# Kernel optimization log

Hardware: AMD Instinct MI355X
Metric: run time of the kernel (lower is better)

The kernel has to match this reference:

```python
import jax, jax.numpy as jnp
import numpy as np
from jax import lax

B, T, L = 256, 128, 64
E_ENC = 512   # encoder_hidden_size
D = 512       # decoder_hidden_size
EMB = 128     # action_embed_size
A = 129       # action_size + 1
ATT_H = 20    # attention MLP hidden width


def setup_inputs() -> dict:
    key = jax.random.key(0)
    ks = jax.random.split(key, 32)
    n = lambda k, shape, s=0.05: jax.random.normal(k, shape, jnp.float32) * s
    inp = {
        'padded_actions': jax.random.randint(ks[0], (B, T), 0, A),
        'sentence_encoding': jax.random.normal(ks[1], (B, L, E_ENC), jnp.float32),
        'enc_h': jax.random.normal(ks[2], (B, D), jnp.float32),
        'enc_c': jax.random.normal(ks[3], (B, D), jnp.float32),
        # embedding
        'emb_W': n(ks[4], (A, EMB)),
        # attn_combine: Linear(E_ENC+EMB -> D)  (cat order: [embed, ctx])
        'Wc': n(ks[5], (D, EMB + E_ENC)), 'bc': jnp.zeros((D,), jnp.float32),
        # three LSTMCells (torch layout: W_ih [4D, in], W_hh [4D, D])
        'Wih1': n(ks[6], (4 * D, D)), 'Whh1': n(ks[7], (4 * D, D)),
        'bih1': jnp.zeros((4 * D,), jnp.float32), 'bhh1': jnp.zeros((4 * D,), jnp.float32),
        'Wih2': n(ks[8], (4 * D, D)), 'Whh2': n(ks[9], (4 * D, D)),
        'bih2': jnp.zeros((4 * D,), jnp.float32), 'bhh2': jnp.zeros((4 * D,), jnp.float32),
        'Wih3': n(ks[10], (4 * D, D)), 'Whh3': n(ks[11], (4 * D, D)),
        'bih3': jnp.zeros((4 * D,), jnp.float32), 'bhh3': jnp.zeros((4 * D,), jnp.float32),
        # attention MLP: Linear(D+E_ENC -> 20), ReLU, Linear(20 -> 1), Tanh
        'Wa1': n(ks[12], (ATT_H, E_ENC + D)), 'ba1': jnp.zeros((ATT_H,), jnp.float32),
        'Wa2': n(ks[13], (1, ATT_H)), 'ba2': jnp.zeros((1,), jnp.float32),
        # action head: Linear(D+E_ENC -> D), ReLU, Linear(D -> A)
        'Wl1': n(ks[14], (D, D + E_ENC)), 'bl1': jnp.zeros((D,), jnp.float32),
        'Wl2': n(ks[15], (A, D)), 'bl2': jnp.zeros((A,), jnp.float32),
    }
    return inp


def _lstm_cell(x, h, c, Wih, Whh, bih, bhh):
    gates = x @ Wih.T + bih + h @ Whh.T + bhh  # [B, 4D]
    i, f, g, o = jnp.split(gates, 4, axis=-1)
    c_new = jax.nn.sigmoid(f) * c + jax.nn.sigmoid(i) * jnp.tanh(g)
    h_new = jax.nn.sigmoid(o) * jnp.tanh(c_new)
    return h_new, c_new


def reference(padded_actions, sentence_encoding, enc_h, enc_c, emb_W, Wc, bc,
              Wih1, Whh1, bih1, bhh1, Wih2, Whh2, bih2, bhh2, Wih3, Whh3, bih3, bhh3,
              Wa1, ba1, Wa2, ba2, Wl1, bl1, Wl2, bl2):
    bsz, tlen = padded_actions.shape
    lmax = sentence_encoding.shape[1]
    embed = emb_W[padded_actions]  # [B, T, EMB]
    # deterministic teacher forcing: embed_tm1 at t is embed[:, t-1], zeros at t=0
    emb_tm1_seq = jnp.concatenate(
        [jnp.zeros((bsz, 1, embed.shape[-1]), embed.dtype), embed[:, :-1]], axis=1)
    xs = jnp.swapaxes(emb_tm1_seq, 0, 1)  # [T, B, EMB]

    ctx0 = jnp.zeros((bsz, sentence_encoding.shape[-1]), jnp.float32)
    init = (enc_h, enc_c, enc_h, enc_c, enc_h, enc_c, ctx0)

    def step(carry, e_tm1):
        h0, c0, h1, c1, h2, c2, ctx = carry
        att_t = jnp.concatenate([e_tm1, ctx], axis=-1) @ Wc.T + bc  # attn_combine
        h0, c0 = _lstm_cell(att_t, h0, c0, Wih1, Whh1, bih1, bhh1)
        h1, c1 = _lstm_cell(h0, h1, c1, Wih2, Whh2, bih2, bhh2)
        h2, c2 = _lstm_cell(h1, h2, c2, Wih3, Whh3, bih3, bhh3)
        # attention over encoder outputs: cat(enc_out, h2) -> MLP -> tanh -> softmax
        h_rep = jnp.broadcast_to(h2[:, None, :], (bsz, lmax, h2.shape[-1]))
        feat = jnp.concatenate([sentence_encoding, h_rep], axis=-1)  # [B, L, E+D]
        score = jnp.tanh(jax.nn.relu(feat @ Wa1.T + ba1) @ Wa2.T + ba2)[..., 0]  # [B, L]
        w = jax.nn.softmax(score, axis=1)
        ctx_new = jnp.einsum('bl,ble->be', w, sentence_encoding)
        # action head on cat(h2, ctx)
        hw = jnp.concatenate([h2, ctx_new], axis=-1)
        logits = jax.nn.relu(hw @ Wl1.T + bl1) @ Wl2.T + bl2  # [B, A]
        return (h0, c0, h1, c1, h2, c2, ctx_new), logits

    _, logits_seq = lax.scan(step, init, xs)  # [T, B, A]
    logits = jnp.swapaxes(logits_seq, 0, 1).reshape(bsz * tlen, -1)
    return logits
```

## Files before the change

kernel.cpp:

```cpp
#include <hip/hip_runtime.h>
#include <math.h>

constexpr int BSZ  = 256;
constexpr int TLEN = 128;
constexpr int LLEN = 64;
constexpr int DH   = 512;
constexpr int EMBD = 128;
constexpr int ACTN = 129;
constexpr int HATT = 20;

typedef short bf16x8 __attribute__((ext_vector_type(8)));
typedef float f32x4  __attribute__((ext_vector_type(4)));

__device__ __forceinline__ short f2bf(float f) {
    unsigned u = __builtin_bit_cast(unsigned, f);
    u += 0x7fffu + ((u >> 16) & 1u);
    return (short)(u >> 16);
}
__device__ __forceinline__ float bf2f(short s) {
    unsigned u = ((unsigned)(unsigned short)s) << 16;
    return __builtin_bit_cast(float, u);
}

__launch_bounds__(256)
__global__ void k_fold(const float* __restrict__ Wih1, const float* __restrict__ Wc,
                       float* __restrict__ W1f)
{
    __shared__ float at[64][33];
    __shared__ float bt[32][65];
    int tid = threadIdx.x;
    int tx = tid & 15, ty = tid >> 4;
    int n0 = blockIdx.x * 64, k0 = blockIdx.y * 64;
    float acc[4][4] = {};
    for (int m0 = 0; m0 < 512; m0 += 32) {
        for (int i = 0; i < 8; ++i) {
            int idx = tid + 256 * i;
            int nl = idx >> 5, ml = idx & 31;
            at[nl][ml] = Wih1[(size_t)(n0 + nl) * 512 + m0 + ml];
        }
        for (int i = 0; i < 8; ++i) {
            int idx = tid + 256 * i;
            int ml = idx >> 6, kl = idx & 63;
            bt[ml][kl] = Wc[(size_t)(m0 + ml) * 640 + k0 + kl];
        }
        __syncthreads();
        for (int m = 0; m < 32; ++m) {
            #pragma unroll
            for (int i = 0; i < 4; ++i) {
                float av = at[ty * 4 + i][m];
                #pragma unroll
                for (int j = 0; j < 4; ++j)
                    acc[i][j] += av * bt[m][tx * 4 + j];
            }
        }
        __syncthreads();
    }
    for (int i = 0; i < 4; ++i)
        for (int j = 0; j < 4; ++j)
            W1f[(size_t)(n0 + ty * 4 + i) * 640 + (k0 + tx * 4 + j)] = acc[i][j];
}

__global__ void k_pack23(const float* __restrict__ Wih, const float* __restrict__ Whh,
                         short* __restrict__ pack)
{
    int idx = blockIdx.x * 256 + threadIdx.x;
    int lane = idx & 63;
    int ks = (idx >> 6) & 31;
    int nn = idx >> 11;
    int np = nn * 16 + (lane & 15);
    int k  = ks * 32 + ((lane >> 4) << 3);
    int n  = (np & 3) * 512 + (np >> 2);
    const float* src = (k < 512) ? (Wih + (size_t)n * 512 + k)
                                 : (Whh + (size_t)n * 512 + (k - 512));
    short* dst = pack + (size_t)idx * 8;
    #pragma unroll
    for (int i = 0; i < 8; ++i) dst[i] = f2bf(src[i]);
}

__global__ void k_pack1(const float* __restrict__ W1f, const float* __restrict__ Whh1,
                        short* __restrict__ pack)
{
    int idx = blockIdx.x * 256 + threadIdx.x;
    int lane = idx & 63;
    int tmp = idx >> 6;
    int ks = tmp % 36;
    int nn = tmp / 36;
    int np = nn * 16 + (lane & 15);
    int k  = ks * 32 + ((lane >> 4) << 3);
    int n  = (np & 3) * 512 + (np >> 2);
    const float* src = (k < 640) ? (W1f + (size_t)n * 640 + k)
                                 : (Whh1 + (size_t)n * 512 + (k - 640));
    short* dst = pack + (size_t)idx * 8;
    #pragma unroll
    for (int i = 0; i < 8; ++i) dst[i] = f2bf(src[i]);
}

__global__ void k_packh1(const float* __restrict__ Wl1, short* __restrict__ pack)
{
    int idx = blockIdx.x * 256 + threadIdx.x;
    int lane = idx & 63;
    int ks = (idx >> 6) & 31;
    int nn = idx >> 11;
    int np = nn * 16 + (lane & 15);
    int k  = ks * 32 + ((lane >> 4) << 3);
    const float* src = Wl1 + (size_t)np * 1024 + k;
    short* dst = pack + (size_t)idx * 8;
    #pragma unroll
    for (int i = 0; i < 8; ++i) dst[i] = f2bf(src[i]);
}

__global__ void k_packh2(const float* __restrict__ Wl2, short* __restrict__ pack)
{
    int idx = blockIdx.x * 256 + threadIdx.x;
    int lane = idx & 63;
    int ks = (idx >> 6) & 15;
    int nn = idx >> 10;
    int np = nn * 16 + (lane & 15);
    int k  = ks * 32 + ((lane >> 4) << 3);
    short* dst = pack + (size_t)idx * 8;
    if (np < ACTN) {
        const float* src = Wl2 + (size_t)np * 512 + k;
        #pragma unroll
        for (int i = 0; i < 8; ++i) dst[i] = f2bf(src[i]);
    } else {
        #pragma unroll
        for (int i = 0; i < 8; ++i) dst[i] = 0;
    }
}

__global__ void k_bias(const float* __restrict__ Wih1, const float* __restrict__ bc,
                       const float* bih1, const float* bhh1,
                       const float* bih2, const float* bhh2,
                       const float* bih3, const float* bhh3,
                       float* b1p, float* b2p, float* b3p)
{
    int cp = blockIdx.x * 256 + threadIdx.x;
    int n = (cp & 3) * 512 + (cp >> 2);
    float s = bih1[n] + bhh1[n];
    for (int m = 0; m < 512; ++m) s += Wih1[(size_t)n * 512 + m] * bc[m];
    b1p[cp] = s;
    b2p[cp] = bih2[n] + bhh2[n];
    b3p[cp] = bih3[n] + bhh3[n];
}

__global__ void k_tr(float* __restrict__ dst, const float* __restrict__ src,
                     int R, int C, int sld, int dld)
{
    int idx = blockIdx.x * 256 + threadIdx.x;
    if (idx >= R * C) return;
    int c = idx / R, r = idx - c * R;
    dst[c * dld + r] = src[r * sld + c];
}

__launch_bounds__(256)
__global__ void k_encp(const float* __restrict__ enc, const float* __restrict__ Wa1,
                       const float* __restrict__ ba1, float* __restrict__ ENCP)
{
    __shared__ float wa[HATT * 513];
    __shared__ float er[8][513];
    int b = blockIdx.x, tid = threadIdx.x;
    for (int idx = tid; idx < HATT * 512; idx += 256) {
        int h = idx >> 9, e = idx & 511;
        wa[h * 513 + e] = Wa1[h * 1024 + e];
    }
    __syncthreads();
    for (int c = 0; c < 8; ++c) {
        for (int i = 0; i < 16; ++i) {
            int idx = tid + 256 * i;
            int rr = idx >> 9, e = idx & 511;
            er[rr][e] = enc[((size_t)b * LLEN + c * 8 + rr) * 512 + e];
        }
        __syncthreads();
        if (tid < 8 * HATT) {
            int rr = tid & 7, h = tid >> 3;
            float s = 0.f;
            for (int e = 0; e < 512; ++e) s += er[rr][e] * wa[h * 513 + e];
            ENCP[((size_t)b * LLEN + c * 8 + rr) * HATT + h] = s + ba1[h];
        }
        __syncthreads();
    }
}

__global__ void k_embed(const int* __restrict__ act, const float* __restrict__ embW,
                        short* __restrict__ ET)
{
    int idx = blockIdx.x * 256 + threadIdx.x;
    int t = idx >> 15;
    int rem = idx & 32767;
    int b = rem >> 7, k = rem & 127;
    float v = 0.f;
    if (t > 0) v = embW[(size_t)act[b * TLEN + t - 1] * EMBD + k];
    ET[idx] = f2bf(v);
}

__global__ void k_encb(const float* __restrict__ enc, short* __restrict__ ENCB)
{
    int i = blockIdx.x * 256 + threadIdx.x;
    float4 v = *(const float4*)&enc[(size_t)i * 4];
    short4 o;
    o.x = f2bf(v.x); o.y = f2bf(v.y); o.z = f2bf(v.z); o.w = f2bf(v.w);
    *(short4*)&ENCB[(size_t)i * 4] = o;
}

__global__ void k_init(const float* __restrict__ eh,
                       short* h0, short* h1, short* h2, short* ctx)
{
    int i = blockIdx.x * 256 + threadIdx.x;
    short hb = f2bf(eh[i]);
    h0[i] = hb; h1[i] = hb; h2[i] = hb; ctx[i] = 0;
}

__device__ __forceinline__ void load_a8(const short* base,
    bf16x8& a0, bf16x8& a1, bf16x8& a2, bf16x8& a3,
    bf16x8& a4, bf16x8& a5, bf16x8& a6, bf16x8& a7)
{
    asm volatile(
        "global_load_dwordx4 %0, %8, off sc0\n\t"
        "global_load_dwordx4 %1, %8, off offset:64 sc0\n\t"
        "global_load_dwordx4 %2, %8, off offset:128 sc0\n\t"
        "global_load_dwordx4 %3, %8, off offset:192 sc0\n\t"
        "global_load_dwordx4 %4, %8, off offset:256 sc0\n\t"
        "global_load_dwordx4 %5, %8, off offset:320 sc0\n\t"
        "global_load_dwordx4 %6, %8, off offset:384 sc0\n\t"
        "global_load_dwordx4 %7, %8, off offset:448 sc0\n\t"
        "s_waitcnt vmcnt(0)"
        : "=&v"(a0), "=&v"(a1), "=&v"(a2), "=&v"(a3),
          "=&v"(a4), "=&v"(a5), "=&v"(a6), "=&v"(a7)
        : "v"(base) : "memory");
    __builtin_amdgcn_sched_barrier(0);
}

__device__ __forceinline__ void load_a4(const short* base,
    bf16x8& a0, bf16x8& a1, bf16x8& a2, bf16x8& a3)
{
    asm volatile(
        "global_load_dwordx4 %0, %4, off sc0\n\t"
        "global_load_dwordx4 %1, %4, off offset:64 sc0\n\t"
        "global_load_dwordx4 %2, %4, off offset:128 sc0\n\t"
        "global_load_dwordx4 %3, %4, off offset:192 sc0\n\t"
        "s_waitcnt vmcnt(0)"
        : "=&v"(a0), "=&v"(a1), "=&v"(a2), "=&v"(a3)
        : "v"(base) : "memory");
    __builtin_amdgcn_sched_barrier(0);
}

__device__ __forceinline__ bf16x8 load_a1(const short* p)
{
    bf16x8 r;
    asm volatile("global_load_dwordx4 %0, %1, off sc0\n\t"
                 "s_waitcnt vmcnt(0)"
                 : "=&v"(r) : "v"(p) : "memory");
    __builtin_amdgcn_sched_barrier(0);
    return r;
}

#define MFMA(af, bf, acc) \
    acc = __builtin_amdgcn_mfma_f32_16x16x32_bf16(af, bf, acc, 0, 0, 0)

__device__ __forceinline__ void lstm_epilogue(
    const float* __restrict__ biasp, float* cstS, short* __restrict__ hout,
    float* gsc, int brow0, int lr, int tid)
{
    __syncthreads();
    int row = tid >> 4, j = tid & 15;
    float4 bv = *(const float4*)&biasp[(lr * 16 + j) * 4];
    float gi = gsc[row * 68 + j * 4 + 0] + bv.x;
    float gf = gsc[row * 68 + j * 4 + 1] + bv.y;
    float gg = gsc[row * 68 + j * 4 + 2] + bv.z;
    float go = gsc[row * 68 + j * 4 + 3] + bv.w;
    float c0 = cstS[tid];
    float si = 1.f / (1.f + __expf(-gi));
    float sf = 1.f / (1.f + __expf(-gf));
    float so = 1.f / (1.f + __expf(-go));
    float cn = sf * c0 + si * tanhf(gg);
    cstS[tid] = cn;
    hout[(size_t)(brow0 + row) * 512 + lr * 16 + j] = f2bf(so * tanhf(cn));
}

__device__ __forceinline__ void lstm1_reg(
    const bf16x8 (&w)[32], int wv, int lane,
    const short* __restrict__ pack1, const short* __restrict__ ET_t,
    const short* __restrict__ ctx, const short* __restrict__ h0old,
    const float* __restrict__ biasp, float* cstS, short* __restrict__ hout,
    float* gsc, int brow0, int lr, int tid)
{
    if (wv < 4) {
        const int rlane = lane & 15, kq = lane >> 4;
        const int ct = lr * 4 + wv;
        f32x4 acc0 = {}, acc1 = {};
        const short* bp = pack1 + ((size_t)(ct * 36) * 64 + lane) * 8;
        #pragma unroll
        for (int ks = 0; ks < 4; ++ks) {
            bf16x8 bf = *(const bf16x8*)(bp + ks * 512);
            bf16x8 af0 = *(const bf16x8*)(ET_t + (size_t)(brow0 + rlane) * EMBD + ks * 32 + kq * 8);
            bf16x8 af1 = *(const bf16x8*)(ET_t + (size_t)(brow0 + 16 + rlane) * EMBD + ks * 32 + kq * 8);
            MFMA(af0, bf, acc0);
            MFMA(af1, bf, acc1);
        }
        #pragma unroll
        for (int c = 0; c < 4; ++c) {
            const short* src = (c < 2) ? ctx : h0old;
            const int krel = (c & 1) * 8;
            const short* ab0 = src + (size_t)(brow0 + rlane) * 512 + krel * 32 + kq * 8;
            const short* ab1 = src + (size_t)(brow0 + 16 + rlane) * 512 + krel * 32 + kq * 8;
            bf16x8 a0, a1, a2, a3, a4, a5, a6, a7;
            load_a8(ab0, a0, a1, a2, a3, a4, a5, a6, a7);
            MFMA(a0, w[c * 8 + 0], acc0); MFMA(a1, w[c * 8 + 1], acc0);
            MFMA(a2, w[c * 8 + 2], acc0); MFMA(a3, w[c * 8 + 3], acc0);
            MFMA(a4, w[c * 8 + 4], acc0); MFMA(a5, w[c * 8 + 5], acc0);
            MFMA(a6, w[c * 8 + 6], acc0); MFMA(a7, w[c * 8 + 7], acc0);
            load_a8(ab1, a0, a1, a2, a3, a4, a5, a6, a7);
            MFMA(a0, w[c * 8 + 0], acc1); MFMA(a1, w[c * 8 + 1], acc1);
            MFMA(a2, w[c * 8 + 2], acc1); MFMA(a3, w[c * 8 + 3], acc1);
            MFMA(a4, w[c * 8 + 4], acc1); MFMA(a5, w[c * 8 + 5], acc1);
            MFMA(a6, w[c * 8 + 6], acc1); MFMA(a7, w[c * 8 + 7], acc1);
        }
        const int rlane2 = lane & 15, kq2 = lane >> 4;
        #pragma unroll
        for (int r = 0; r < 4; ++r) {
            gsc[(kq2 * 4 + r) * 68 + wv * 16 + rlane2] = acc0[r];
            gsc[(16 + kq2 * 4 + r) * 68 + wv * 16 + rlane2] = acc1[r];
        }
    }
    lstm_epilogue(biasp, cstS, hout, gsc, brow0, lr, tid);
}

__device__ __forceinline__ void lstm3_reg(
    const bf16x8 (&w)[32], int wv, int lane,
    const short* __restrict__ s1, const short* __restrict__ s2,
    const float* __restrict__ biasp, float* cstS, short* __restrict__ hout,
    float* gsc, int brow0, int lr, int tid)
{
    if (wv >= 4) {
        const int cw = wv - 4;
        const int rlane = lane & 15, kq = lane >> 4;
        f32x4 acc0 = {}, acc1 = {};
        #pragma unroll
        for (int c = 0; c < 4; ++c) {
            const short* src = (c < 2) ? s1 : s2;
            const int krel = (c & 1) * 8;
            const short* ab0 = src + (size_t)(brow0 + rlane) * 512 + krel * 32 + kq * 8;
            const short* ab1 = src + (size_t)(brow0 + 16 + rlane) * 512 + krel * 32 + kq * 8;
            bf16x8 a0, a1, a2, a3, a4, a5, a6, a7;
            load_a8(ab0, a0, a1, a2, a3, a4, a5, a6, a7);
            MFMA(a0, w[c * 8 + 0], acc0); MFMA(a1, w[c * 8 + 1], acc0);
            MFMA(a2, w[c * 8 + 2], acc0); MFMA(a3, w[c * 8 + 3], acc0);
            MFMA(a4, w[c * 8 + 4], acc0); MFMA(a5, w[c * 8 + 5], acc0);
            MFMA(a6, w[c * 8 + 6], acc0); MFMA(a7, w[c * 8 + 7], acc0);
            load_a8(ab1, a0, a1, a2, a3, a4, a5, a6, a7);
            MFMA(a0, w[c * 8 + 0], acc1); MFMA(a1, w[c * 8 + 1], acc1);
            MFMA(a2, w[c * 8 + 2], acc1); MFMA(a3, w[c * 8 + 3], acc1);
            MFMA(a4, w[c * 8 + 4], acc1); MFMA(a5, w[c * 8 + 5], acc1);
            MFMA(a6, w[c * 8 + 6], acc1); MFMA(a7, w[c * 8 + 7], acc1);
        }
        #pragma unroll
        for (int r = 0; r < 4; ++r) {
            gsc[(kq * 4 + r) * 68 + cw * 16 + rlane] = acc0[r];
            gsc[(16 + kq * 4 + r) * 68 + cw * 16 + rlane] = acc1[r];
        }
    }
    lstm_epilogue(biasp, cstS, hout, gsc, brow0, lr, tid);
}

__device__ __forceinline__ void lstm2_lds(
    const short* wlds, const short* __restrict__ s1, const short* __restrict__ s2,
    const float* __restrict__ biasp, float* cstS, short* __restrict__ hout,
    float* gsc, int brow0, int lr, int tid)
{
    const int wave = tid >> 6, lane = tid & 63;
    const int wm = wave >> 2, wn = wave & 3;
    const int rlane = lane & 15, kq = lane >> 4;
    const int arow = brow0 + wm * 16 + rlane;
    f32x4 acc = {};
    #pragma unroll
    for (int c = 0; c < 4; ++c) {
        const int kss = c * 8;
        const short* src = (kss < 16) ? s1 : s2;
        const int krel = kss & 15;
        const short* abase = src + (size_t)arow * 512 + krel * 32 + kq * 8;
        const short* wb = wlds + ((wn * 32 + kss) * 64 + lane) * 8;
        bf16x8 b0 = *(const bf16x8*)(wb + 0 * 512);
        bf16x8 b1 = *(const bf16x8*)(wb + 1 * 512);
        bf16x8 b2 = *(const bf16x8*)(wb + 2 * 512);
        bf16x8 b3 = *(const bf16x8*)(wb + 3 * 512);
        bf16x8 b4 = *(const bf16x8*)(wb + 4 * 512);
        bf16x8 b5 = *(const bf16x8*)(wb + 5 * 512);
        bf16x8 b6 = *(const bf16x8*)(wb + 6 * 512);
        bf16x8 b7 = *(const bf16x8*)(wb + 7 * 512);
        bf16x8 a0, a1, a2, a3, a4, a5, a6, a7;
        load_a8(abase, a0, a1, a2, a3, a4, a5, a6, a7);
        MFMA(a0, b0, acc); MFMA(a1, b1, acc); MFMA(a2, b2, acc); MFMA(a3, b3, acc);
        MFMA(a4, b4, acc); MFMA(a5, b5, acc); MFMA(a6, b6, acc); MFMA(a7, b7, acc);
    }
    #pragma unroll
    for (int r = 0; r < 4; ++r)
        gsc[(wm * 16 + kq * 4 + r) * 68 + wn * 16 + rlane] = acc[r];
    lstm_epilogue(biasp, cstS, hout, gsc, brow0, lr, tid);
}

__device__ __forceinline__ void head1_stage(
    const short* __restrict__ ph1, const float* __restrict__ bl1,
    const short* __restrict__ h2q, const short* __restrict__ ctx,
    short* __restrict__ hidden, float* gsc, int brow0, int lr, int tid)
{
    const int wave = tid >> 6, lane = tid & 63;
    const int wm = wave & 1, kq2 = wave >> 1;
    const int rlane = lane & 15, kq = lane >> 4;
    const int arow = brow0 + wm * 16 + rlane;
    const short* src = (kq2 < 2) ? h2q : ctx;
    const int krel = (kq2 & 1) * 8;
    const short* abase = src + (size_t)arow * 512 + krel * 32 + kq * 8;
    const short* wb = ph1 + ((size_t)(lr * 32 + kq2 * 8) * 64 + lane) * 8;
    f32x4 acc = {};
    #pragma unroll
    for (int g = 0; g < 2; ++g) {
        bf16x8 b0 = *(const bf16x8*)(wb + (g * 4 + 0) * 512);
        bf16x8 b1 = *(const bf16x8*)(wb + (g * 4 + 1) * 512);
        bf16x8 b2 = *(const bf16x8*)(wb + (g * 4 + 2) * 512);
        bf16x8 b3 = *(const bf16x8*)(wb + (g * 4 + 3) * 512);
        bf16x8 a0, a1, a2, a3;
        load_a4(abase + g * 128, a0, a1, a2, a3);
        MFMA(a0, b0, acc); MFMA(a1, b1, acc); MFMA(a2, b2, acc); MFMA(a3, b3, acc);
    }
    #pragma unroll
    for (int r = 0; r < 4; ++r)
        gsc[(kq2 * 2 + wm) * 256 + (kq * 4 + r) * 16 + rlane] = acc[r];
    __syncthreads();
    {
        float s = 0.f;
        #pragma unroll
        for (int k = 0; k < 4; ++k) s += gsc[(k * 2 + (tid >> 8)) * 256 + (tid & 255)];
        int row = (tid >> 8) * 16 + ((tid >> 4) & 15);
        int col = lr * 16 + (tid & 15);
        hidden[(size_t)(brow0 + row) * 512 + col] = f2bf(fmaxf(s + bl1[col], 0.f));
    }
    __syncthreads();
}

__device__ __forceinline__ void head2_stage(
    const short* __restrict__ ph2, const float* __restrict__ bl2,
    const short* __restrict__ hidden, float* __restrict__ out, int t,
    float* gsc, int brow0, int nt, int tid)
{
    const int wave = tid >> 6, lane = tid & 63;
    const int wm = wave & 1, kq4 = wave >> 1;
    const int rlane = lane & 15, kq = lane >> 4;
    const int arow = brow0 + wm * 16 + rlane;
    const short* abase = hidden + (size_t)arow * 512 + kq4 * 128 + kq * 8;
    const short* wb = ph2 + ((size_t)(nt * 16 + kq4 * 4) * 64 + lane) * 8;
    bf16x8 b0 = *(const bf16x8*)(wb + 0 * 512);
    bf16x8 b1 = *(const bf16x8*)(wb + 1 * 512);
    bf16x8 b2 = *(const bf16x8*)(wb + 2 * 512);
    bf16x8 b3 = *(const bf16x8*)(wb + 3 * 512);
    bf16x8 a0, a1, a2, a3;
    load_a4(abase, a0, a1, a2, a3);
    f32x4 acc = {};
    MFMA(a0, b0, acc); MFMA(a1, b1, acc); MFMA(a2, b2, acc); MFMA(a3, b3, acc);
    #pragma unroll
    for (int r = 0; r < 4; ++r)
        gsc[(kq4 * 2 + wm) * 256 + (kq * 4 + r) * 16 + rlane] = acc[r];
    __syncthreads();
    {
        float s = 0.f;
        #pragma unroll
        for (int k = 0; k < 4; ++k) s += gsc[(k * 2 + (tid >> 8)) * 256 + (tid & 255)];
        int row = (tid >> 8) * 16 + ((tid >> 4) & 15);
        int col = nt * 16 + (tid & 15);
        if (col < ACTN)
            out[((size_t)(brow0 + row) * TLEN + t) * ACTN + col] = s + bl2[col];
    }
}

__device__ __forceinline__ void attn_stage(
    const short* __restrict__ h2q, const short* __restrict__ ENCB,
    const float* __restrict__ ENCP, const float* __restrict__ WaHT,
    const float* __restrict__ Wa2, const float* __restrict__ ba2v,
    short* __restrict__ ctx,
    float* h2s, float* part, float* hp, float* sl, int b, int tid)
{
    if (tid < 64) {
        bf16x8 v = load_a1(h2q + (size_t)b * 512 + tid * 8);
        #pragma unroll
        for (int i = 0; i < 8; ++i) h2s[tid * 8 + i] = bf2f(v[i]);
    }
    __syncthreads();
    if (tid < 8 * HATT) {
        int h = tid % HATT, sg = tid / HATT;
        float s = 0.f;
        for (int e = sg * 64; e < sg * 64 + 64; ++e) s += h2s[e] * WaHT[e * HATT + h];
        part[sg * HATT + h] = s;
    }
    __syncthreads();
    if (tid < HATT) {
        float s = 0.f;
        #pragma unroll
        for (int sg = 0; sg < 8; ++sg) s += part[sg * HATT + tid];
        hp[tid] = s;
    }
    __syncthreads();
    if (tid < LLEN) {
        float s = ba2v[0];
        const float* ep = ENCP + ((size_t)b * LLEN + tid) * HATT;
        #pragma unroll
        for (int h = 0; h < HATT; ++h)
            s += fmaxf(ep[h] + hp[h], 0.f) * Wa2[h];
        float v = tanhf(s);
        float m = v;
        for (int o = 32; o; o >>= 1) m = fmaxf(m, __shfl_xor(m, o));
        float e = __expf(v - m);
        float ss = e;
        for (int o = 32; o; o >>= 1) ss += __shfl_xor(ss, o);
        sl[tid] = e / ss;
    }
    __syncthreads();
    {
        float a = 0.f;
        const short* eb = ENCB + (size_t)b * LLEN * 512 + tid;
        #pragma unroll 8
        for (int l = 0; l < LLEN; ++l) a += sl[l] * bf2f(eb[l * 512]);
        ctx[(size_t)b * 512 + tid] = f2bf(a);
    }
    __syncthreads();
}

__launch_bounds__(512)
__global__ void k_mega(
    const short* __restrict__ pack1, const short* __restrict__ pack2,
    const short* __restrict__ pack3, const short* __restrict__ ph1,
    const short* __restrict__ ph2,
    const float* __restrict__ b1p, const float* __restrict__ b2p,
    const float* __restrict__ b3p, const float* __restrict__ bl1,
    const float* __restrict__ bl2,
    const short* __restrict__ ET, const short* __restrict__ ENCB,
    const float* __restrict__ ENCP, const float* __restrict__ WaHT,
    const float* __restrict__ Wa2, const float* __restrict__ ba2v,
    const float* __restrict__ enc_c,
    short* __restrict__ h0a, short* __restrict__ h0b,
    short* __restrict__ h1a, short* __restrict__ h1b,
    short* __restrict__ h2a, short* __restrict__ h2b,
    short* __restrict__ ctx, short* __restrict__ hidden,
    int* __restrict__ cnt, unsigned long long* __restrict__ bar,
    float* __restrict__ out)
{
    __shared__ __align__(16) short wlds[65536];
    __shared__ float gsc[2176];
    __shared__ float cst[3 * 512];
    __shared__ float h2s[512];
    __shared__ float part[8 * HATT];
    __shared__ float hp[HATT];
    __shared__ float sl[LLEN];
    __shared__ int sinfo[2];

    const int tid = threadIdx.x;
    const int wv = tid >> 6, lane = tid & 63;

    int xcd_reg;
    asm volatile("s_getreg_b32 %0, hwreg(HW_REG_XCC_ID)" : "=s"(xcd_reg));
    if (tid == 0) {
        sinfo[0] = xcd_reg;
        sinfo[1] = __hip_atomic_fetch_add(&cnt[xcd_reg], 1,
                                          __ATOMIC_RELAXED, __HIP_MEMORY_SCOPE_AGENT);
    }
    __syncthreads();
    const int myx = sinfo[0], lr = sinfo[1];
    const int brow0 = myx * 32;

    {
        const bf16x8* s2v = (const bf16x8*)(pack2 + (size_t)lr * 65536);
        bf16x8* dst = (bf16x8*)wlds;
        for (int i = tid; i < 8192; i += 512)
            dst[i] = __builtin_nontemporal_load(&s2v[i]);
    }
    bf16x8 wreg[32];
    {
        const short* wsrc = (wv < 4)
            ? pack1 + ((size_t)((lr * 4 + wv) * 36 + 4) * 64 + lane) * 8
            : pack3 + ((size_t)((lr * 4 + (wv - 4)) * 32) * 64 + lane) * 8;
        #pragma unroll
        for (int i = 0; i < 32; ++i)
            wreg[i] = *(const bf16x8*)(wsrc + (size_t)i * 512);
    }
    {
        int row = tid >> 4, j = tid & 15;
        float cv = enc_c[(size_t)(brow0 + row) * 512 + lr * 16 + j];
        cst[tid] = cv; cst[512 + tid] = cv; cst[1024 + tid] = cv;
    }
    __syncthreads();

    int gen = 0;
    unsigned long long* mybar = &bar[myx * 16];
    auto gbar = [&]() {
        ++gen;
        asm volatile("s_waitcnt vmcnt(0)" ::: "memory");
        __syncthreads();
        if (tid == 0) {
            __hip_atomic_fetch_add(mybar, 1ull,
                                   __ATOMIC_RELAXED, __HIP_MEMORY_SCOPE_AGENT);
            const unsigned long long target = 32ull * (unsigned long long)gen;
            while (__hip_atomic_load(mybar, __ATOMIC_RELAXED,
                                     __HIP_MEMORY_SCOPE_AGENT) < target)
                __builtin_amdgcn_s_sleep(2);
        }
        __syncthreads();
    };

    short* h0p[2] = { h0a, h0b };
    short* h1p[2] = { h1a, h1b };
    short* h2p[2] = { h2a, h2b };
    const int b_att = brow0 + lr;

    for (int t = 0; t < TLEN; ++t) {
        int p = t & 1, q = p ^ 1;
        lstm1_reg(wreg, wv, lane, pack1, ET + (size_t)t * BSZ * EMBD,
                  ctx, h0p[p], b1p, cst, h0p[q], gsc, brow0, lr, tid);
        gbar();
        lstm2_lds(wlds, h0p[q], h1p[p], b2p, cst + 512, h1p[q],
                  gsc, brow0, lr, tid);
        gbar();
        lstm3_reg(wreg, wv, lane, h1p[q], h2p[p], b3p, cst + 1024, h2p[q],
                  gsc, brow0, lr, tid);
        gbar();
        attn_stage(h2p[q], ENCB, ENCP, WaHT, Wa2, ba2v, ctx,
                   h2s, part, hp, sl, b_att, tid);
        if (t > 0 && lr >= 9 && lr < 18)
            head2_stage(ph2, bl2, hidden, out, t - 1, gsc, brow0, lr - 9, tid);
        gbar();
        head1_stage(ph1, bl1, h2p[q], ctx, hidden, gsc, brow0, lr, tid);
    }
    gbar();
    if (lr >= 9 && lr < 18)
        head2_stage(ph2, bl2, hidden, out, TLEN - 1, gsc, brow0, lr - 9, tid);
}

extern "C" void kernel_launch(void* const* d_in, const int* in_sizes, int n_in,
                              void* d_out, int out_size, void* d_ws, size_t ws_size,
                              hipStream_t stream)
{
    const int*   act   = (const int*)d_in[0];
    const float* enc   = (const float*)d_in[1];
    const float* enc_h = (const float*)d_in[2];
    const float* enc_c = (const float*)d_in[3];
    const float* embW  = (const float*)d_in[4];
    const float* Wc    = (const float*)d_in[5];
    const float* bc    = (const float*)d_in[6];
    const float* Wih1  = (const float*)d_in[7];
    const float* Whh1  = (const float*)d_in[8];
    const float* bih1  = (const float*)d_in[9];
    const float* bhh1  = (const float*)d_in[10];
    const float* Wih2  = (const float*)d_in[11];
    const float* Whh2  = (const float*)d_in[12];
    const float* bih2  = (const float*)d_in[13];
    const float* bhh2  = (const float*)d_in[14];
    const float* Wih3  = (const float*)d_in[15];
    const float* Whh3  = (const float*)d_in[16];
    const float* bih3  = (const float*)d_in[17];
    const float* bhh3  = (const float*)d_in[18];
    const float* Wa1   = (const float*)d_in[19];
    const float* ba1   = (const float*)d_in[20];
    const float* Wa2   = (const float*)d_in[21];
    const float* ba2   = (const float*)d_in[22];
    const float* Wl1   = (const float*)d_in[23];
    const float* bl1   = (const float*)d_in[24];
    const float* Wl2   = (const float*)d_in[25];
    const float* bl2   = (const float*)d_in[26];
    float* out = (float*)d_out;

    char* cur = (char*)d_ws;
    auto alloc = [&](size_t bytes) {
        char* p = cur;
        cur += (bytes + 255) & ~(size_t)255;
        return p;
    };
    int* cnt = (int*)alloc(64);
    unsigned long long* bar = (unsigned long long*)alloc(8 * 16 * 8);
    short* pack1  = (short*)alloc((size_t)2048 * 1152 * 2);
    short* pack2  = (short*)alloc((size_t)2048 * 1024 * 2);
    short* pack3  = (short*)alloc((size_t)2048 * 1024 * 2);
    short* packh1 = (short*)alloc((size_t)512 * 1024 * 2);
    short* packh2 = (short*)alloc((size_t)192 * 512 * 2);
    short* ENCB   = (short*)alloc((size_t)BSZ * LLEN * 512 * 2);
    float* W1f    = (float*)ENCB;
    float* b1p    = (float*)alloc(2048 * 4);
    float* b2p    = (float*)alloc(2048 * 4);
    float* b3p    = (float*)alloc(2048 * 4);
    float* WaHT   = (float*)alloc(512 * HATT * 4);
    float* ENCP   = (float*)alloc((size_t)BSZ * LLEN * HATT * 4);
    short* ET     = (short*)alloc((size_t)TLEN * BSZ * EMBD * 2);
    const size_t SB = (size_t)BSZ * DH;
    short* h0a = (short*)alloc(SB * 2); short* h0b = (short*)alloc(SB * 2);
    short* h1a = (short*)alloc(SB * 2); short* h1b = (short*)alloc(SB * 2);
    short* h2a = (short*)alloc(SB * 2); short* h2b = (short*)alloc(SB * 2);
    short* ctx    = (short*)alloc(SB * 2);
    short* hidden = (short*)alloc(SB * 2);

    hipMemsetAsync(cnt, 0, 64, stream);
    hipMemsetAsync(bar, 0, 8 * 16 * 8, stream);
    k_fold<<<dim3(32, 10), 256, 0, stream>>>(Wih1, Wc, W1f);
    k_pack1<<<1152, 256, 0, stream>>>(W1f, Whh1, pack1);
    k_encb<<<8192, 256, 0, stream>>>(enc, ENCB);
    k_pack23<<<1024, 256, 0, stream>>>(Wih2, Whh2, pack2);
    k_pack23<<<1024, 256, 0, stream>>>(Wih3, Whh3, pack3);
    k_packh1<<<256, 256, 0, stream>>>(Wl1, packh1);
    k_packh2<<<48, 256, 0, stream>>>(Wl2, packh2);
    k_bias<<<8, 256, 0, stream>>>(Wih1, bc, bih1, bhh1, bih2, bhh2, bih3, bhh3,
                                  b1p, b2p, b3p);
    k_tr<<<(HATT * 512 + 255) / 256, 256, 0, stream>>>(WaHT, Wa1 + 512, HATT, 512, 1024, HATT);
    k_encp<<<BSZ, 256, 0, stream>>>(enc, Wa1, ba1, ENCP);
    k_embed<<<(TLEN * BSZ * EMBD) / 256, 256, 0, stream>>>(act, embW, ET);
    k_init<<<512, 256, 0, stream>>>(enc_h, h0a, h1a, h2a, ctx);

    k_mega<<<256, 512, 0, stream>>>(
        pack1, pack2, pack3, packh1, packh2,
        b1p, b2p, b3p, bl1, bl2,
        ET, ENCB, ENCP, WaHT, Wa2, ba2,
        enc_c,
        h0a, h0b, h1a, h1b, h2a, h2b,
        ctx, hidden, cnt, bar, out);
}
```

Before: 9.863 ms.

## Replace atomic-counter grid barrier with per-block flag slots and cache encoder rows in registers

The per-XCD grid barrier changes from a single atomic counter polled by one thread to per-block generation slots. Each block stores its own flag, and one wavefront polls all 32 slots in parallel with a wave-wide vote, which avoids atomic contention on one cache line. Each block's attention rows of the bf16 encoder output are now loaded into registers once before the time loop, so the context reduction no longer re-reads global memory every step. The cost is higher register pressure (64 more shorts per thread) on top of the 32 bf16x8 weight registers already held, with a possible spill risk.

```diff
diff --git a/kernel.cpp b/kernel.cpp
--- a/kernel.cpp
+++ b/kernel.cpp
@@ -315,11 +315,10 @@
             MFMA(a4, w[c * 8 + 4], acc1); MFMA(a5, w[c * 8 + 5], acc1);
             MFMA(a6, w[c * 8 + 6], acc1); MFMA(a7, w[c * 8 + 7], acc1);
         }
-        const int rlane2 = lane & 15, kq2 = lane >> 4;
         #pragma unroll
         for (int r = 0; r < 4; ++r) {
-            gsc[(kq2 * 4 + r) * 68 + wv * 16 + rlane2] = acc0[r];
-            gsc[(16 + kq2 * 4 + r) * 68 + wv * 16 + rlane2] = acc1[r];
+            gsc[(kq * 4 + r) * 68 + wv * 16 + rlane] = acc0[r];
+            gsc[(16 + kq * 4 + r) * 68 + wv * 16 + rlane] = acc1[r];
         }
     }
     lstm_epilogue(biasp, cstS, hout, gsc, brow0, lr, tid);
@@ -472,7 +471,7 @@
 }
 
 __device__ __forceinline__ void attn_stage(
-    const short* __restrict__ h2q, const short* __restrict__ ENCB,
+    const short* __restrict__ h2q, const bf16x8 (&encR)[8],
     const float* __restrict__ ENCP, const float* __restrict__ WaHT,
     const float* __restrict__ Wa2, const float* __restrict__ ba2v,
     short* __restrict__ ctx,
@@ -515,9 +514,11 @@
     __syncthreads();
     {
         float a = 0.f;
-        const short* eb = ENCB + (size_t)b * LLEN * 512 + tid;
-        #pragma unroll 8
-        for (int l = 0; l < LLEN; ++l) a += sl[l] * bf2f(eb[l * 512]);
+        #pragma unroll
+        for (int i = 0; i < 8; ++i)
+            #pragma unroll
+            for (int j = 0; j < 8; ++j)
+                a += sl[i * 8 + j] * bf2f(encR[i][j]);
         ctx[(size_t)b * 512 + tid] = f2bf(a);
     }
     __syncthreads();
@@ -539,7 +540,7 @@
     short* __restrict__ h1a, short* __restrict__ h1b,
     short* __restrict__ h2a, short* __restrict__ h2b,
     short* __restrict__ ctx, short* __restrict__ hidden,
-    int* __restrict__ cnt, unsigned long long* __restrict__ bar,
+    int* __restrict__ cnt, unsigned* __restrict__ bar,
     float* __restrict__ out)
 {
     __shared__ __align__(16) short wlds[65536];
@@ -580,6 +581,17 @@
         for (int i = 0; i < 32; ++i)
             wreg[i] = *(const bf16x8*)(wsrc + (size_t)i * 512);
     }
+    bf16x8 encR[8];
+    {
+        const short* ebase = ENCB + ((size_t)(brow0 + lr) * LLEN) * 512 + tid;
+        #pragma unroll
+        for (int i = 0; i < 8; ++i) {
+            bf16x8 v;
+            #pragma unroll
+            for (int j = 0; j < 8; ++j) v[j] = ebase[(size_t)(i * 8 + j) * 512];
+            encR[i] = v;
+        }
+    }
     {
         int row = tid >> 4, j = tid & 15;
         float cv = enc_c[(size_t)(brow0 + row) * 512 + lr * 16 + j];
@@ -587,19 +599,25 @@
     }
     __syncthreads();
 
-    int gen = 0;
-    unsigned long long* mybar = &bar[myx * 16];
+    unsigned gen = 0;
+    unsigned* myslot = &bar[(myx * 32 + lr) * 16];
+    unsigned* xslots = &bar[(size_t)myx * 32 * 16];
     auto gbar = [&]() {
         ++gen;
         asm volatile("s_waitcnt vmcnt(0)" ::: "memory");
         __syncthreads();
-        if (tid == 0) {
-            __hip_atomic_fetch_add(mybar, 1ull,
-                                   __ATOMIC_RELAXED, __HIP_MEMORY_SCOPE_AGENT);
-            const unsigned long long target = 32ull * (unsigned long long)gen;
-            while (__hip_atomic_load(mybar, __ATOMIC_RELAXED,
-                                     __HIP_MEMORY_SCOPE_AGENT) < target)
+        if (tid == 0)
+            __hip_atomic_store(myslot, gen, __ATOMIC_RELAXED,
+                               __HIP_MEMORY_SCOPE_AGENT);
+        if (tid < 64) {
+            for (;;) {
+                unsigned v = 0xFFFFFFFFu;
+                if (tid < 32)
+                    v = __hip_atomic_load(&xslots[tid * 16], __ATOMIC_RELAXED,
+                                          __HIP_MEMORY_SCOPE_AGENT);
+                if (__all(v >= gen)) break;
                 __builtin_amdgcn_s_sleep(2);
+            }
         }
         __syncthreads();
     };
@@ -620,7 +638,7 @@
         lstm3_reg(wreg, wv, lane, h1p[q], h2p[p], b3p, cst + 1024, h2p[q],
                   gsc, brow0, lr, tid);
         gbar();
-        attn_stage(h2p[q], ENCB, ENCP, WaHT, Wa2, ba2v, ctx,
+        attn_stage(h2p[q], encR, ENCP, WaHT, Wa2, ba2v, ctx,
                    h2s, part, hp, sl, b_att, tid);
         if (t > 0 && lr >= 9 && lr < 18)
             head2_stage(ph2, bl2, hidden, out, t - 1, gsc, brow0, lr - 9, tid);
@@ -672,7 +690,7 @@
         return p;
     };
     int* cnt = (int*)alloc(64);
-    unsigned long long* bar = (unsigned long long*)alloc(8 * 16 * 8);
+    unsigned* bar = (unsigned*)alloc(8 * 32 * 16 * 4);
     short* pack1  = (short*)alloc((size_t)2048 * 1152 * 2);
     short* pack2  = (short*)alloc((size_t)2048 * 1024 * 2);
     short* pack3  = (short*)alloc((size_t)2048 * 1024 * 2);
@@ -694,7 +712,7 @@
     short* hidden = (short*)alloc(SB * 2);
 
     hipMemsetAsync(cnt, 0, 64, stream);
-    hipMemsetAsync(bar, 0, 8 * 16 * 8, stream);
+    hipMemsetAsync(bar, 0, 8 * 32 * 16 * 4, stream);
     k_fold<<<dim3(32, 10), 256, 0, stream>>>(Wih1, Wc, W1f);
     k_pack1<<<1152, 256, 0, stream>>>(W1f, Whh1, pack1);
     k_encb<<<8192, 256, 0, stream>>>(enc, ENCB);
```

Measured after the change: 10.25 ms. 3.9% more time.
